# Optimization experiments

Measured on AMD Instinct MI355X. Metric: run time of the kernel, lower is better.

Reference implementation:

```python
import jax, jax.numpy as jnp
import numpy as np

N0, N1, N2, N3 = 524288, 262144, 65536, 8192
E0, E1, E2 = 2621440, 655360, 81920
D_IN, D_H, D_OUT = 256, 256, 64


def setup_inputs() -> dict:
    key = jax.random.key(0)
    ks = jax.random.split(key, 16)
    s = 0.02
    inp = {
        "x": jax.random.normal(ks[0], (N0, D_IN), dtype=jnp.float32),
        "src0": jax.random.randint(ks[1], (E0,), 0, N0, dtype=jnp.int32),
        "dst0": jax.random.randint(ks[2], (E0,), 0, N1, dtype=jnp.int32),
        "src1": jax.random.randint(ks[3], (E1,), 0, N1, dtype=jnp.int32),
        "dst1": jax.random.randint(ks[4], (E1,), 0, N2, dtype=jnp.int32),
        "src2": jax.random.randint(ks[5], (E2,), 0, N2, dtype=jnp.int32),
        "dst2": jax.random.randint(ks[6], (E2,), 0, N3, dtype=jnp.int32),
        "nd0": N1, "nd1": N2, "nd2": N3,
        "Wfc": jax.random.normal(ks[7], (D_IN, D_H), dtype=jnp.float32) * s,
        "bfc": jnp.zeros((D_H,), dtype=jnp.float32),
        "Ws0": jax.random.normal(ks[8], (D_H, D_H), dtype=jnp.float32) * s,
        "Wn0": jax.random.normal(ks[9], (D_H, D_H), dtype=jnp.float32) * s,
        "b0": jnp.zeros((D_H,), dtype=jnp.float32),
        "Ws1": jax.random.normal(ks[10], (D_H, D_H), dtype=jnp.float32) * s,
        "Wn1": jax.random.normal(ks[11], (D_H, D_H), dtype=jnp.float32) * s,
        "b1": jnp.zeros((D_H,), dtype=jnp.float32),
        "Ws2": jax.random.normal(ks[12], (D_H, D_OUT), dtype=jnp.float32) * s,
        "Wn2": jax.random.normal(ks[13], (D_H, D_OUT), dtype=jnp.float32) * s,
        "b2": jnp.zeros((D_OUT,), dtype=jnp.float32),
    }
    return inp


def sage_conv(h, src, dst, n_dst, Ws, Wn, b):
    # DGL SAGEConv 'mean': out = h_dst @ W_self + mean_neigh(h_src) @ W_neigh + b
    h_dst = h[:n_dst]
    msg = jnp.take(h, src, axis=0)                    # [E, d] gather
    agg = jax.ops.segment_sum(msg, dst, num_segments=n_dst)
    cnt = jax.ops.segment_sum(jnp.ones((dst.shape[0],), h.dtype), dst, num_segments=n_dst)
    mean = agg / jnp.maximum(cnt, 1.0)[:, None]
    return h_dst @ Ws + mean @ Wn + b


def reference(x, src0, dst0, src1, dst1, src2, dst2, nd0, nd1, nd2,
              Wfc, bfc, Ws0, Wn0, b0, Ws1, Wn1, b1, Ws2, Wn2, b2):
    h = jax.nn.relu(x @ Wfc + bfc)                    # input projection (dropout=0 -> identity)
    h = jax.nn.relu(sage_conv(h, src0, dst0, nd0, Ws0, Wn0, b0))
    h = jax.nn.relu(sage_conv(h, src1, dst1, nd1, Ws1, Wn1, b1))
    h = sage_conv(h, src2, dst2, nd2, Ws2, Wn2, b2)   # no activation on final layer
    return h
```

## Files before the change

kernel.cpp:

```cpp
#include <hip/hip_runtime.h>

constexpr int N0c = 524288, N1c = 262144, N2c = 65536, N3c = 8192;
constexpr int NTOT = N1c + N2c + N3c;

typedef __attribute__((ext_vector_type(8))) short   bf16x8;
typedef __attribute__((ext_vector_type(4))) float   f32x4;
typedef __attribute__((ext_vector_type(8))) unsigned short u16x8;

__device__ inline unsigned short f2bf(float f) {
    union { float f; unsigned u; } v; v.f = f;
    unsigned r = v.u + 0x7FFF + ((v.u >> 16) & 1);
    return (unsigned short)(r >> 16);
}
__device__ inline float bf2f(unsigned short u) {
    union { unsigned u; float f; } v; v.u = ((unsigned)u) << 16;
    return v.f;
}

__device__ inline void glds16(const void* g, void* l) {
    __builtin_amdgcn_global_load_lds(
        (const __attribute__((address_space(1))) unsigned int*)g,
        (__attribute__((address_space(3))) unsigned int*)l, 16, 0, 0);
}

struct WPack { const float* w[7]; unsigned short* o[7]; };

__global__ __launch_bounds__(256)
void wconv_all(WPack p)
{
    const int idx = blockIdx.x * 256 + threadIdx.x;
    int widx, off, N;
    if (idx < 327680) { widx = idx >> 16; off = idx & 65535; N = 256; }
    else {
        const int r = idx - 327680;
        widx = 5 + (r >> 14); off = r & 16383; N = 64;
        if (widx > 6) return;
    }
    const int k = off / N, n = off % N;
    p.o[widx][n * 256 + k] = f2bf(p.w[widx][off]);
}

__device__ inline bf16x8 pack_bf8(const float* p) {
    const f32x4 u = *(const f32x4*)p;
    const f32x4 v = *(const f32x4*)(p + 4);
    bf16x8 t;
    #pragma unroll
    for (int j = 0; j < 4; ++j) {
        t[j]     = (short)f2bf(u[j]);
        t[j + 4] = (short)f2bf(v[j]);
    }
    return t;
}

template<int NT, int KC, bool DUAL, bool RELU, bool A_F32, bool OUT_BF16>
__global__ __launch_bounds__(512, 2)
void gemm2(const void* __restrict__ A1v, const void* __restrict__ A2v,
           const unsigned short* __restrict__ Wt1,
           const unsigned short* __restrict__ Wt2,
           const float* __restrict__ bias, void* __restrict__ Cv)
{
    constexpr int N     = NT * 16;
    constexpr int PH    = 256 / KC;
    constexpr int SLOTS = KC / 8;
    constexpr int GPM   = N * SLOTS;
    constexpr int TOTG  = GPM * (DUAL ? 2 : 1);
    static_assert(TOTG == 4096, "LDS sizing");
    __shared__ unsigned short Bs[TOTG * 8];

    const int t    = threadIdx.x;
    const int lane = t & 63;
    const int wv   = t >> 6;
    const int col  = lane & 15;
    const int kg   = lane >> 4;
    const int swz  = (col & 7) << 3;
    const long row0 = (long)blockIdx.x * 128 + wv * 16;

    const unsigned short* A1h = (const unsigned short*)A1v;
    const float*          A1f = (const float*)A1v;
    const unsigned short* A2h = (const unsigned short*)A2v;

    f32x4 acc[NT];
    #pragma unroll
    for (int nt = 0; nt < NT; ++nt) acc[nt] = (f32x4){0.f, 0.f, 0.f, 0.f};

    const long ar = (row0 + col) * 256;

    for (int kh = 0; kh < PH; ++kh) {
        if (kh) __syncthreads();
        #pragma unroll
        for (int it = 0; it < TOTG / 512; ++it) {
            const int g  = it * 512 + t;
            const int m  = DUAL ? (g / GPM) : 0;
            const int gm = DUAL ? (g % GPM) : g;
            const int n  = gm / SLOTS;
            const int s  = gm % SLOTS;
            const int ss = s ^ (n & 7);
            const unsigned short* srcb =
                (m ? Wt2 : Wt1) + n * 256 + kh * KC + ss * 8;
            glds16(srcb, &Bs[(it * 512 + wv * 64) * 8]);
        }
        __syncthreads();

        #pragma unroll
        for (int k0 = 0; k0 < KC; k0 += 32) {
            const int kx = (k0 + kg * 8) ^ swz;
            const long ac = ar + kh * KC + k0 + kg * 8;
            bf16x8 a1, a2;
            if constexpr (A_F32) a1 = pack_bf8(&A1f[ac]);
            else                 a1 = *(const bf16x8*)&A1h[ac];
            if constexpr (DUAL)  a2 = *(const bf16x8*)&A2h[ac];
            #pragma unroll
            for (int nt = 0; nt < NT; ++nt) {
                const bf16x8 b1 = *(const bf16x8*)&Bs[(nt * 16 + col) * KC + kx];
                acc[nt] = __builtin_amdgcn_mfma_f32_16x16x32_bf16(a1, b1, acc[nt], 0, 0, 0);
                if constexpr (DUAL) {
                    const bf16x8 b2 = *(const bf16x8*)&Bs[GPM * 8 + (nt * 16 + col) * KC + kx];
                    acc[nt] = __builtin_amdgcn_mfma_f32_16x16x32_bf16(a2, b2, acc[nt], 0, 0, 0);
                }
            }
        }
    }

    #pragma unroll
    for (int nt = 0; nt < NT; ++nt) {
        const int c = nt * 16 + col;
        const float bb = bias[c];
        #pragma unroll
        for (int rr = 0; rr < 4; ++rr) {
            const long row = row0 + kg * 4 + rr;
            float o = acc[nt][rr] + bb;
            if constexpr (RELU) o = fmaxf(o, 0.f);
            if constexpr (OUT_BF16)
                ((unsigned short*)Cv)[row * N + c] = f2bf(o);
            else
                ((float*)Cv)[row * N + c] = o;
        }
    }
}

struct CsrArgs {
    const int* src0; const int* dst0;
    const int* src1; const int* dst1;
    const int* src2; const int* dst2;
    int e0, e01, etot;
};

__global__ __launch_bounds__(256)
void hist_all(CsrArgs a, int* __restrict__ hist)
{
    const int i = blockIdx.x * 256 + threadIdx.x;
    if (i >= a.etot) return;
    const int* dstp; int e, hb;
    if (i < a.e0)       { dstp = a.dst0; e = i;         hb = 0; }
    else if (i < a.e01) { dstp = a.dst1; e = i - a.e0;  hb = N1c; }
    else                { dstp = a.dst2; e = i - a.e01; hb = N1c + N2c; }
    atomicAdd(&hist[hb + dstp[e]], 1);
}

__global__ __launch_bounds__(256)
void scan1_k(const int* __restrict__ hist, int* __restrict__ offs,
             int* __restrict__ bsum, int n)
{
    __shared__ int sm[256];
    const int t = threadIdx.x;
    const int base = blockIdx.x * 1024 + t * 4;
    int4 v = make_int4(0, 0, 0, 0);
    if (base < n) v = *(const int4*)&hist[base];
    const int s = v.x + v.y + v.z + v.w;
    int val = s;
    sm[t] = val; __syncthreads();
    #pragma unroll
    for (int off = 1; off < 256; off <<= 1) {
        const int add = (t >= off) ? sm[t - off] : 0;
        __syncthreads();
        val += add;
        sm[t] = val;
        __syncthreads();
    }
    const int excl = val - s;
    if (base < n) {
        offs[base]     = excl;
        offs[base + 1] = excl + v.x;
        offs[base + 2] = excl + v.x + v.y;
        offs[base + 3] = excl + v.x + v.y + v.z;
    }
    if (t == 255) bsum[blockIdx.x] = val;
}

__global__ __launch_bounds__(512)
void scan2_k(int* __restrict__ bsum, int nb)
{
    __shared__ int sm[512];
    const int t = threadIdx.x;
    const int s = (t < nb) ? bsum[t] : 0;
    int val = s;
    sm[t] = val; __syncthreads();
    #pragma unroll
    for (int off = 1; off < 512; off <<= 1) {
        const int add = (t >= off) ? sm[t - off] : 0;
        __syncthreads();
        val += add;
        sm[t] = val;
        __syncthreads();
    }
    if (t < nb) bsum[t] = val - s;
}

__global__ __launch_bounds__(256)
void scan3_k(int* __restrict__ offs, const int* __restrict__ bsum, int etot)
{
    const int i = blockIdx.x * 256 + threadIdx.x;
    offs[i] += bsum[i >> 10];
    if (i == 0) offs[NTOT] = etot;
}

__global__ __launch_bounds__(256)
void fill_all(CsrArgs a, const int* __restrict__ offs, int* __restrict__ hist,
              int* __restrict__ ssrc)
{
    const int i = blockIdx.x * 256 + threadIdx.x;
    if (i >= a.etot) return;
    const int* dstp; const int* srcp; int e, hb;
    if (i < a.e0)       { dstp = a.dst0; srcp = a.src0; e = i;         hb = 0; }
    else if (i < a.e01) { dstp = a.dst1; srcp = a.src1; e = i - a.e0;  hb = N1c; }
    else                { dstp = a.dst2; srcp = a.src2; e = i - a.e01; hb = N1c + N2c; }
    const int g = hb + dstp[e];
    const int p = atomicAdd(&hist[g], -1) - 1;
    ssrc[offs[g] + p] = srcp[e];
}

__global__ __launch_bounds__(256)
void agg_k(const unsigned short* __restrict__ h, const int* __restrict__ ssrc,
           const int* __restrict__ ob, unsigned short* __restrict__ agg, int n)
{
    const int w    = blockIdx.x * 4 + (threadIdx.x >> 6);
    const int lane = threadIdx.x & 63;
    if (w >= n) return;
    const int beg = ob[w];
    const int end = ob[w + 1];
    const int hf  = lane >> 5;
    const int co  = (lane & 31) * 8;

    float acc[8] = {0.f, 0.f, 0.f, 0.f, 0.f, 0.f, 0.f, 0.f};

    for (int j = beg; j < end; j += 16) {
        u16x8 v[8];
        bool  ok[8];
        #pragma unroll
        for (int q = 0; q < 8; ++q) {
            const int e  = j + 2 * q + hf;
            ok[q] = (e < end);
            const int es = ok[q] ? e : (end - 1);
            v[q] = *(const u16x8*)&h[(size_t)ssrc[es] * 256 + co];
        }
        #pragma unroll
        for (int q = 0; q < 8; ++q)
            #pragma unroll
            for (int c = 0; c < 8; ++c)
                acc[c] += ok[q] ? bf2f(v[q][c]) : 0.0f;
    }

    #pragma unroll
    for (int c = 0; c < 8; ++c) acc[c] += __shfl_xor(acc[c], 32);

    if (hf == 0) {
        const float inv = 1.0f / fmaxf((float)(end - beg), 1.0f);
        u16x8 o;
        #pragma unroll
        for (int c = 0; c < 8; ++c) o[c] = f2bf(acc[c] * inv);
        *(u16x8*)&agg[(size_t)w * 256 + co] = o;
    }
}

extern "C" void kernel_launch(void* const* d_in, const int* in_sizes, int n_in,
                              void* d_out, int out_size, void* d_ws, size_t ws_size,
                              hipStream_t stream)
{
    const float* x    = (const float*)d_in[0];
    const int*   src0 = (const int*)d_in[1];
    const int*   dst0 = (const int*)d_in[2];
    const int*   src1 = (const int*)d_in[3];
    const int*   dst1 = (const int*)d_in[4];
    const int*   src2 = (const int*)d_in[5];
    const int*   dst2 = (const int*)d_in[6];
    const float* Wfc  = (const float*)d_in[10];
    const float* bfc  = (const float*)d_in[11];
    const float* Ws0  = (const float*)d_in[12];
    const float* Wn0  = (const float*)d_in[13];
    const float* b0   = (const float*)d_in[14];
    const float* Ws1  = (const float*)d_in[15];
    const float* Wn1  = (const float*)d_in[16];
    const float* b1   = (const float*)d_in[17];
    const float* Ws2  = (const float*)d_in[18];
    const float* Wn2  = (const float*)d_in[19];
    const float* b2   = (const float*)d_in[20];
    const int E0 = in_sizes[1], E1 = in_sizes[3], E2 = in_sizes[5];
    const int Etot = E0 + E1 + E2;

    char* ws = (char*)d_ws;
    unsigned short* h0   = (unsigned short*)ws;
    unsigned short* h1   = (unsigned short*)(ws + (256ULL << 20));
    unsigned short* h2   = (unsigned short*)(ws + (384ULL << 20));
    unsigned short* agg  = (unsigned short*)(ws + (416ULL << 20));
    unsigned short* Wt   = (unsigned short*)(ws + (544ULL << 20));
    int*            hist = (int*)(ws + (545ULL << 20));
    int*            offs = (int*)(ws + (547ULL << 20));
    int*            bsum = (int*)(ws + (549ULL << 20));
    int*            ssrc = (int*)(ws + (550ULL << 20));

    unsigned short* wfc = Wt;
    unsigned short* ws0 = Wt + 65536;
    unsigned short* wn0 = Wt + 131072;
    unsigned short* ws1 = Wt + 196608;
    unsigned short* wn1 = Wt + 262144;
    unsigned short* ws2 = Wt + 327680;
    unsigned short* wn2 = Wt + 344064;

    const dim3 blk(256);

    WPack wp;
    wp.w[0] = Wfc; wp.w[1] = Ws0; wp.w[2] = Wn0; wp.w[3] = Ws1; wp.w[4] = Wn1;
    wp.w[5] = Ws2; wp.w[6] = Wn2;
    wp.o[0] = wfc; wp.o[1] = ws0; wp.o[2] = wn0; wp.o[3] = ws1; wp.o[4] = wn1;
    wp.o[5] = ws2; wp.o[6] = wn2;
    wconv_all<<<dim3(1408), blk, 0, stream>>>(wp);

    CsrArgs ca;
    ca.src0 = src0; ca.dst0 = dst0; ca.src1 = src1; ca.dst1 = dst1;
    ca.src2 = src2; ca.dst2 = dst2;
    ca.e0 = E0; ca.e01 = E0 + E1; ca.etot = Etot;
    hipMemsetAsync(hist, 0, (size_t)NTOT * 4, stream);
    hist_all<<<dim3((Etot + 255) / 256), blk, 0, stream>>>(ca, hist);
    scan1_k<<<dim3(NTOT / 1024), blk, 0, stream>>>(hist, offs, bsum, NTOT);
    scan2_k<<<dim3(1), dim3(512), 0, stream>>>(bsum, NTOT / 1024);
    scan3_k<<<dim3(NTOT / 256), blk, 0, stream>>>(offs, bsum, Etot);
    fill_all<<<dim3((Etot + 255) / 256), blk, 0, stream>>>(ca, offs, hist, ssrc);

    gemm2<16, 128, false, true, true, true><<<dim3(N0c / 128), dim3(512), 0, stream>>>(
        x, nullptr, wfc, nullptr, bfc, h0);

    agg_k<<<dim3(N1c / 4), blk, 0, stream>>>(h0, ssrc, offs, agg, N1c);
    gemm2<16, 64, true, true, false, true><<<dim3(N1c / 128), dim3(512), 0, stream>>>(
        h0, agg, ws0, wn0, b0, h1);

    agg_k<<<dim3(N2c / 4), blk, 0, stream>>>(h1, ssrc, offs + N1c, agg, N2c);
    gemm2<16, 64, true, true, false, true><<<dim3(N2c / 128), dim3(512), 0, stream>>>(
        h1, agg, ws1, wn1, b1, h2);

    agg_k<<<dim3(N3c / 4), blk, 0, stream>>>(h2, ssrc, offs + N1c + N2c, agg, N3c);
    gemm2<4, 256, true, false, false, false><<<dim3(N3c / 128), dim3(512), 0, stream>>>(
        h2, agg, ws2, wn2, b2, (float*)d_out);
}
```

Before: 937.8 us.

## Record atomic ranks during histogram, drop second atomic pass; split agg tail loop

The histogram kernel now stores each edge's atomic return value as its rank. The fill kernel then writes sorted sources without a second atomic decrement pass, so atomics on the histogram happen only once. Zeroing of the histogram is folded into the weight-conversion kernel, replacing the memset. The aggregation loop gets an unpredicated main body with separate tail handling. The cost is an extra rank array of about 3.3M ints, written once and read back once.

```diff
diff --git a/kernel.cpp b/kernel.cpp
--- a/kernel.cpp
+++ b/kernel.cpp
@@ -26,8 +26,13 @@
 struct WPack { const float* w[7]; unsigned short* o[7]; };
 
 __global__ __launch_bounds__(256)
-void wconv_all(WPack p)
-{
+void wconv_all(WPack p, int* __restrict__ hist)
+{
+    if (blockIdx.x >= 1408) {
+        const int zid = (blockIdx.x - 1408) * 256 + threadIdx.x;
+        ((int4*)hist)[zid] = make_int4(0, 0, 0, 0);
+        return;
+    }
     const int idx = blockIdx.x * 256 + threadIdx.x;
     int widx, off, N;
     if (idx < 327680) { widx = idx >> 16; off = idx & 65535; N = 256; }
@@ -146,7 +151,7 @@
 };
 
 __global__ __launch_bounds__(256)
-void hist_all(CsrArgs a, int* __restrict__ hist)
+void rank_k(CsrArgs a, int* __restrict__ hist, int* __restrict__ rank)
 {
     const int i = blockIdx.x * 256 + threadIdx.x;
     if (i >= a.etot) return;
@@ -154,7 +159,7 @@
     if (i < a.e0)       { dstp = a.dst0; e = i;         hb = 0; }
     else if (i < a.e01) { dstp = a.dst1; e = i - a.e0;  hb = N1c; }
     else                { dstp = a.dst2; e = i - a.e01; hb = N1c + N2c; }
-    atomicAdd(&hist[hb + dstp[e]], 1);
+    rank[i] = atomicAdd(&hist[hb + dstp[e]], 1);
 }
 
 __global__ __launch_bounds__(256)
@@ -215,8 +220,8 @@
 }
 
 __global__ __launch_bounds__(256)
-void fill_all(CsrArgs a, const int* __restrict__ offs, int* __restrict__ hist,
-              int* __restrict__ ssrc)
+void place_k(CsrArgs a, const int* __restrict__ offs, const int* __restrict__ rank,
+             int* __restrict__ ssrc)
 {
     const int i = blockIdx.x * 256 + threadIdx.x;
     if (i >= a.etot) return;
@@ -225,8 +230,7 @@
     else if (i < a.e01) { dstp = a.dst1; srcp = a.src1; e = i - a.e0;  hb = N1c; }
     else                { dstp = a.dst2; srcp = a.src2; e = i - a.e01; hb = N1c + N2c; }
     const int g = hb + dstp[e];
-    const int p = atomicAdd(&hist[g], -1) - 1;
-    ssrc[offs[g] + p] = srcp[e];
+    ssrc[offs[g] + rank[i]] = srcp[e];
 }
 
 __global__ __launch_bounds__(256)
@@ -243,21 +247,42 @@
 
     float acc[8] = {0.f, 0.f, 0.f, 0.f, 0.f, 0.f, 0.f, 0.f};
 
-    for (int j = beg; j < end; j += 16) {
+    int j = beg;
+    for (; j + 16 <= end; j += 16) {
         u16x8 v[8];
-        bool  ok[8];
-        #pragma unroll
-        for (int q = 0; q < 8; ++q) {
-            const int e  = j + 2 * q + hf;
-            ok[q] = (e < end);
-            const int es = ok[q] ? e : (end - 1);
-            v[q] = *(const u16x8*)&h[(size_t)ssrc[es] * 256 + co];
-        }
+        #pragma unroll
+        for (int q = 0; q < 8; ++q)
+            v[q] = *(const u16x8*)&h[(size_t)ssrc[j + 2 * q + hf] * 256 + co];
         #pragma unroll
         for (int q = 0; q < 8; ++q)
             #pragma unroll
-            for (int c = 0; c < 8; ++c)
-                acc[c] += ok[q] ? bf2f(v[q][c]) : 0.0f;
+            for (int c = 0; c < 8; ++c) acc[c] += bf2f(v[q][c]);
+    }
+    const int rem = end - j;
+    if (rem > 8) {
+        u16x8 v[8]; bool ok[8];
+        #pragma unroll
+        for (int q = 0; q < 8; ++q) {
+            const int e = j + 2 * q + hf;
+            ok[q] = (e < end);
+            v[q] = *(const u16x8*)&h[(size_t)ssrc[ok[q] ? e : (end - 1)] * 256 + co];
+        }
+        #pragma unroll
+        for (int q = 0; q < 8; ++q)
+            #pragma unroll
+            for (int c = 0; c < 8; ++c) acc[c] += ok[q] ? bf2f(v[q][c]) : 0.0f;
+    } else if (rem > 0) {
+        u16x8 v[4]; bool ok[4];
+        #pragma unroll
+        for (int q = 0; q < 4; ++q) {
+            const int e = j + 2 * q + hf;
+            ok[q] = (e < end);
+            v[q] = *(const u16x8*)&h[(size_t)ssrc[ok[q] ? e : (end - 1)] * 256 + co];
+        }
+        #pragma unroll
+        for (int q = 0; q < 4; ++q)
+            #pragma unroll
+            for (int c = 0; c < 8; ++c) acc[c] += ok[q] ? bf2f(v[q][c]) : 0.0f;
     }
 
     #pragma unroll
@@ -307,6 +332,7 @@
     int*            offs = (int*)(ws + (547ULL << 20));
     int*            bsum = (int*)(ws + (549ULL << 20));
     int*            ssrc = (int*)(ws + (550ULL << 20));
+    int*            rank = (int*)(ws + (564ULL << 20));
 
     unsigned short* wfc = Wt;
     unsigned short* ws0 = Wt + 65536;
@@ -323,18 +349,17 @@
     wp.w[5] = Ws2; wp.w[6] = Wn2;
     wp.o[0] = wfc; wp.o[1] = ws0; wp.o[2] = wn0; wp.o[3] = ws1; wp.o[4] = wn1;
     wp.o[5] = ws2; wp.o[6] = wn2;
-    wconv_all<<<dim3(1408), blk, 0, stream>>>(wp);
+    wconv_all<<<dim3(1408 + 328), blk, 0, stream>>>(wp, hist);
 
     CsrArgs ca;
     ca.src0 = src0; ca.dst0 = dst0; ca.src1 = src1; ca.dst1 = dst1;
     ca.src2 = src2; ca.dst2 = dst2;
     ca.e0 = E0; ca.e01 = E0 + E1; ca.etot = Etot;
-    hipMemsetAsync(hist, 0, (size_t)NTOT * 4, stream);
-    hist_all<<<dim3((Etot + 255) / 256), blk, 0, stream>>>(ca, hist);
+    rank_k<<<dim3((Etot + 255) / 256), blk, 0, stream>>>(ca, hist, rank);
     scan1_k<<<dim3(NTOT / 1024), blk, 0, stream>>>(hist, offs, bsum, NTOT);
     scan2_k<<<dim3(1), dim3(512), 0, stream>>>(bsum, NTOT / 1024);
     scan3_k<<<dim3(NTOT / 256), blk, 0, stream>>>(offs, bsum, Etot);
-    fill_all<<<dim3((Etot + 255) / 256), blk, 0, stream>>>(ca, offs, hist, ssrc);
+    place_k<<<dim3((Etot + 255) / 256), blk, 0, stream>>>(ca, offs, rank, ssrc);
 
     gemm2<16, 128, false, true, true, true><<<dim3(N0c / 128), dim3(512), 0, stream>>>(
         x, nullptr, wfc, nullptr, bfc, h0);
```

New measurement: 850.7 us. 1.1x faster.
